# Kernel optimization log

Hardware: AMD Instinct MI355X
Metric: run time of the kernel (lower is better)

Reference implementation:

```python
import jax, jax.numpy as jnp
import numpy as np

D_MODEL = 1024
NUM_HEADS = 16
D_K = D_MODEL // NUM_HEADS
THETA = 10000.0
MAX_SEQ_LEN = 2048
BATCH = 2
SEQ = 2048


def setup_inputs() -> dict:
    key = jax.random.key(0)
    ks = jax.random.split(key, 5)
    std = np.sqrt(2.0 / (D_MODEL + D_MODEL)).astype(np.float32)
    x = jax.random.normal(ks[0], (BATCH, SEQ, D_MODEL), dtype=jnp.float32)
    Wq = jax.random.normal(ks[1], (D_MODEL, D_MODEL), dtype=jnp.float32) * std
    Wk = jax.random.normal(ks[2], (D_MODEL, D_MODEL), dtype=jnp.float32) * std
    Wv = jax.random.normal(ks[3], (D_MODEL, D_MODEL), dtype=jnp.float32) * std
    Wo = jax.random.normal(ks[4], (D_MODEL, D_MODEL), dtype=jnp.float32) * std
    token_positions = jnp.arange(SEQ, dtype=jnp.int32)
    return {"x": x, "token_positions": token_positions,
            "Wq": Wq, "Wk": Wk, "Wv": Wv, "Wo": Wo}


def _rope_tables(positions):
    # freqs: [d_k/2]; angles: [seq, d_k/2]
    freqs = 1.0 / (THETA ** (jnp.arange(0, D_K, 2, dtype=jnp.float32) / D_K))
    angles = positions.astype(jnp.float32)[:, None] * freqs[None, :]
    return jnp.cos(angles), jnp.sin(angles)


def _apply_rope(t, cos, sin):
    # t: [b, h, s, d_k]; cos/sin: [s, d_k/2]; interleaved pair rotation
    x1 = t[..., 0::2]
    x2 = t[..., 1::2]
    r1 = x1 * cos - x2 * sin
    r2 = x1 * sin + x2 * cos
    return jnp.stack([r1, r2], axis=-1).reshape(t.shape)


def reference(x, token_positions, Wq, Wk, Wv, Wo):
    b, s, _ = x.shape
    # projections: y = x W^T
    q = jnp.einsum('bsi,oi->bso', x, Wq)
    k = jnp.einsum('bsi,oi->bso', x, Wk)
    v = jnp.einsum('bsi,oi->bso', x, Wv)
    # split heads: [b, h, s, d]
    q = q.reshape(b, s, NUM_HEADS, D_K).transpose(0, 2, 1, 3)
    k = k.reshape(b, s, NUM_HEADS, D_K).transpose(0, 2, 1, 3)
    v = v.reshape(b, s, NUM_HEADS, D_K).transpose(0, 2, 1, 3)
    cos, sin = _rope_tables(token_positions)
    q = _apply_rope(q, cos, sin)
    k = _apply_rope(k, cos, sin)
    scale = jnp.asarray(D_K, jnp.float32) ** 0.5
    scores = jnp.einsum('bhqd,bhkd->bhqk', q, k) / scale
    causal = jnp.tril(jnp.ones((s, s), dtype=bool))
    scores = jnp.where(causal, scores, -jnp.inf)
    attn = jax.nn.softmax(scores.astype(jnp.float32), axis=-1).astype(scores.dtype)
    out = jnp.einsum('bhqk,bhkd->bhqd', attn, v)
    out = out.transpose(0, 2, 1, 3).reshape(b, s, D_MODEL)
    return jnp.einsum('bsi,oi->bso', out, Wo)
```

## Files before the change

kernel.cpp:

```cpp
#include <hip/hip_runtime.h>
#include <stdint.h>

#define D_MODEL 1024
#define NH      16
#define DKH     64
#define SEQLEN  2048
#define BATCH   2
#define KDIM    1024

typedef __attribute__((ext_vector_type(8))) short          short8;
typedef __attribute__((ext_vector_type(4))) short          bf16x4;
typedef __attribute__((ext_vector_type(8))) unsigned short ushort8;
typedef __attribute__((ext_vector_type(4))) unsigned short usht4;
typedef __attribute__((ext_vector_type(4))) float          f32x4;

#define QSCALE 0.18033688011112042f

__device__ __forceinline__ unsigned short f2bf(float f) {
    union { float f; unsigned u; } v; v.f = f;
    unsigned u = v.u;
    unsigned r = (u + 0x7FFFu + ((u >> 16) & 1u)) >> 16;
    return (unsigned short)r;
}
__device__ __forceinline__ unsigned fbits(float f) {
    union { float f; unsigned u; } v; v.f = f; return v.u;
}

__device__ __forceinline__ void gload_lds16(const unsigned short* g, unsigned short* l) {
    __builtin_amdgcn_global_load_lds(
        (__attribute__((address_space(1))) void*)(g),
        (__attribute__((address_space(3))) void*)(l), 16, 0, 0);
}

__global__ void cvt_all(const float* __restrict__ X,  const float* __restrict__ Wq,
                        const float* __restrict__ Wk, const float* __restrict__ Wv,
                        const float* __restrict__ Wo, const int* __restrict__ pos,
                        unsigned short* __restrict__ Xb,  unsigned short* __restrict__ Wqb,
                        unsigned short* __restrict__ Wkb, unsigned short* __restrict__ Wvb,
                        unsigned short* __restrict__ Wob, float2* __restrict__ tbl) {
    const int z = blockIdx.y;
    if (z == 5) {
        int i = blockIdx.x * 256 + threadIdx.x;
        if (i < 65536) {
            int s = i >> 5, j = i & 31;
            float freq = expf(-((float)(2 * j) * (1.0f / 64.0f)) * 9.210340371976184f);
            float ang = (float)pos[s] * freq;
            float sn, cn;
            sincosf(ang, &sn, &cn);
            tbl[i] = make_float2(cn, sn);
        }
        return;
    }
    const float* src; unsigned short* dst; int n;
    if (z == 0)      { src = X;  dst = Xb;  n = 4194304; }
    else if (z == 1) { src = Wq; dst = Wqb; n = 1048576; }
    else if (z == 2) { src = Wk; dst = Wkb; n = 1048576; }
    else if (z == 3) { src = Wv; dst = Wvb; n = 1048576; }
    else             { src = Wo; dst = Wob; n = 1048576; }
    int i = (blockIdx.x * 256 + threadIdx.x) * 8;
    if (i >= n) return;
    float4 a = *(const float4*)(src + i);
    float4 b = *(const float4*)(src + i + 4);
    ushort8 o;
    o[0] = f2bf(a.x); o[1] = f2bf(a.y); o[2] = f2bf(a.z); o[3] = f2bf(a.w);
    o[4] = f2bf(b.x); o[5] = f2bf(b.y); o[6] = f2bf(b.z); o[7] = f2bf(b.w);
    *(ushort8*)(dst + i) = o;
}

__device__ __forceinline__ void gemm_core_128(
    const unsigned short* __restrict__ A, const unsigned short* __restrict__ W,
    unsigned short* a_lds, unsigned short* b_lds,
    int m0, int n0, f32x4 acc[4][4])
{
    const int tid  = threadIdx.x;
    const int lane = tid & 63;
    const int w    = tid >> 6;
    const int quad = lane >> 4;
    const int l16  = lane & 15;
    const int wm   = w & 1, wn = w >> 1;

    const int row_in = lane >> 3;
    const int cg     = ((lane & 7) ^ row_in) * 8;

    #pragma unroll
    for (int mi = 0; mi < 4; mi++)
        #pragma unroll
        for (int ni = 0; ni < 4; ni++) {
            f32x4 z = {0.f, 0.f, 0.f, 0.f};
            acc[mi][ni] = z;
        }

    const int x7 = l16 & 7;

    for (int kk = 0; kk < KDIM; kk += 64) {
        __syncthreads();
        #pragma unroll
        for (int j = 0; j < 4; ++j) {
            int c = w * 4 + j;
            gload_lds16(A + (size_t)(m0 + c * 8 + row_in) * KDIM + kk + cg, &a_lds[c * 512]);
            gload_lds16(W + (size_t)(n0 + c * 8 + row_in) * KDIM + kk + cg, &b_lds[c * 512]);
        }
        __syncthreads();

        short8 af[2][4], bf[2][4];
        #pragma unroll
        for (int kk2 = 0; kk2 < 2; kk2++)
            #pragma unroll
            for (int i = 0; i < 4; i++) {
                int g = (kk2 * 4 + quad) ^ x7;
                af[kk2][i] = *(const short8*)&a_lds[(wm * 64 + i * 16 + l16) * 64 + g * 8];
                bf[kk2][i] = *(const short8*)&b_lds[(wn * 64 + i * 16 + l16) * 64 + g * 8];
            }
        #pragma unroll
        for (int kk2 = 0; kk2 < 2; kk2++)
            #pragma unroll
            for (int mi = 0; mi < 4; mi++)
                #pragma unroll
                for (int ni = 0; ni < 4; ni++)
                    acc[mi][ni] = __builtin_amdgcn_mfma_f32_16x16x32_bf16(af[kk2][mi], bf[kk2][ni], acc[mi][ni], 0, 0, 0);
    }
}

__global__ __launch_bounds__(256, 2)
void gemm_qkv(const unsigned short* __restrict__ X,
              const unsigned short* __restrict__ Wq,
              const unsigned short* __restrict__ Wk,
              const unsigned short* __restrict__ Wv,
              const float2* __restrict__ tbl,
              unsigned short* __restrict__ q_ws,
              unsigned short* __restrict__ k_ws,
              unsigned short* __restrict__ v_ws)
{
    __shared__ __align__(16) unsigned short a_lds[128 * 64];
    __shared__ __align__(16) unsigned short b_lds[128 * 64];
    __shared__ __align__(16) unsigned short t_lds[32 * 136];

    const int z = blockIdx.z;
    const unsigned short* W = (z == 0) ? Wq : ((z == 1) ? Wk : Wv);
    const int m0 = blockIdx.x * 128, n0 = blockIdx.y * 128;

    f32x4 acc[4][4];
    gemm_core_128(X, W, a_lds, b_lds, m0, n0, acc);

    const int tid  = threadIdx.x;
    const int lane = tid & 63;
    const int w    = tid >> 6;
    const int quad = lane >> 4;
    const int l16  = lane & 15;
    const int wm   = w & 1, wn = w >> 1;

    if (z == 2) {
        const int bx = m0 >> 11;
        const int c_local_w = wn * 16 + l16;
        const int rd_c = tid >> 3;
        const int rd_s = (tid & 7) * 16;
        #pragma unroll
        for (int ni = 0; ni < 4; ni++) {
            __syncthreads();
            #pragma unroll
            for (int mi = 0; mi < 4; mi++) {
                usht4 v4;
                #pragma unroll
                for (int r = 0; r < 4; r++) v4[r] = f2bf(acc[mi][ni][r]);
                *(usht4*)&t_lds[c_local_w * 136 + wm * 64 + mi * 16 + quad * 4] = v4;
            }
            __syncthreads();
            int col = n0 + (rd_c >> 4) * 64 + ni * 16 + (rd_c & 15);
            int h = col >> 6, d = col & 63;
            size_t base = (size_t)(bx * NH + h) * DKH * SEQLEN + (size_t)d * SEQLEN
                        + (m0 & 2047) + rd_s;
            ushort8 x0 = *(ushort8*)&t_lds[rd_c * 136 + rd_s];
            ushort8 x1 = *(ushort8*)&t_lds[rd_c * 136 + rd_s + 8];
            *(ushort8*)&v_ws[base]     = x0;
            *(ushort8*)&v_ws[base + 8] = x1;
        }
    } else {
        unsigned short* dst = (z == 0) ? q_ws : k_ws;
        const float sc = (z == 0) ? QSCALE : 1.0f;
        #pragma unroll
        for (int mi = 0; mi < 4; mi++)
            #pragma unroll
            for (int ni = 0; ni < 4; ni++)
                #pragma unroll
                for (int r = 0; r < 4; r++) {
                    int row = m0 + wm * 64 + mi * 16 + quad * 4 + r;
                    int col = n0 + wn * 64 + ni * 16 + l16;
                    int b = row >> 11, s = row & 2047;
                    int h = col >> 6,  d = col & 63;
                    float val = acc[mi][ni][r];
                    float other = __shfl_xor(val, 1);
                    float2 cs = tbl[s * 32 + (d >> 1)];
                    float rv = (d & 1) ? (other * cs.y + val * cs.x)
                                       : (val * cs.x - other * cs.y);
                    dst[(size_t)(b * NH + h) * SEQLEN * DKH + (size_t)s * DKH + d] =
                        f2bf(rv * sc);
                }
    }
}

__global__ __launch_bounds__(512, 2)
void attn_kernel(const unsigned short* __restrict__ q_ws,
                 const unsigned short* __restrict__ k_ws,
                 const unsigned short* __restrict__ v_ws,
                 unsigned short* __restrict__ ao)
{
    __shared__ __align__(16) unsigned short smem[17920];
    unsigned short* k_lds = smem;
    unsigned short* v_lds = smem + 128 * 72;
    float* redO = (float*)smem;
    float* redL = redO + 8192;

    const int bh  = blockIdx.x;
    const int y   = blockIdx.y;
    const int qt2 = (y < 8) ? y : (23 - y);
    const int tid = threadIdx.x, lane = tid & 63, w = tid >> 6;
    const int quad = lane >> 4, l16 = lane & 15;
    const int g   = w >> 2;
    const int w4  = w & 3;
    const int nf0 = g * 4;

    const size_t kqbase = (size_t)bh * SEQLEN * DKH;
    const size_t vbase  = (size_t)bh * DKH * SEQLEN;
    const int b = bh >> 4, h = bh & 15;

    const int krow = tid >> 3, kcol = (tid & 7) * 8;
    const int vrow = tid >> 4, vcol = (tid & 15) * 8;

    const int q0  = qt2 * 128;
    const int nt  = qt2 + 1;
    const int qwbase = q0 + w4 * 32;

    short8 aq[2][2];
    #pragma unroll
    for (int st = 0; st < 2; st++)
        #pragma unroll
        for (int kc = 0; kc < 2; kc++)
            aq[st][kc] = *(const short8*)(q_ws + kqbase +
                (size_t)(qwbase + st * 16 + l16) * DKH + kc * 32 + quad * 8);

    f32x4 o_acc[2][4];
    #pragma unroll
    for (int st = 0; st < 2; st++)
        #pragma unroll
        for (int df = 0; df < 4; df++) { f32x4 z = {0.f,0.f,0.f,0.f}; o_acc[st][df] = z; }
    float lsum[2] = {0.f, 0.f};

    ushort8 kreg[2], vreg[2];
    #pragma unroll
    for (int rr = 0; rr < 2; ++rr) {
        kreg[rr] = *(const ushort8*)(k_ws + kqbase + (size_t)(krow + rr * 64) * DKH + kcol);
        vreg[rr] = *(const ushort8*)(v_ws + vbase + (size_t)(vrow + rr * 32) * SEQLEN + vcol);
    }

    for (int t = 0; t < nt; ++t) {
        const int s0 = t * 128;
        __syncthreads();
        #pragma unroll
        for (int rr = 0; rr < 2; ++rr) {
            *(ushort8*)&k_lds[(krow + rr * 64) * 72 + kcol]  = kreg[rr];
            *(ushort8*)&v_lds[(vrow + rr * 32) * 136 + vcol] = vreg[rr];
        }
        __syncthreads();
        if (t < nt - 1) {
            int s1 = s0 + 128;
            #pragma unroll
            for (int rr = 0; rr < 2; ++rr) {
                kreg[rr] = *(const ushort8*)(k_ws + kqbase + (size_t)(s1 + krow + rr * 64) * DKH + kcol);
                vreg[rr] = *(const ushort8*)(v_ws + vbase + (size_t)(vrow + rr * 32) * SEQLEN + s1 + vcol);
            }
        }

        const bool diag = (t == nt - 1);
        #pragma unroll
        for (int nfi = 0; nfi < 4; nfi++) {
            const int nf = nf0 + nfi;
            short8 kf0 = *(const short8*)&k_lds[(nf * 16 + l16) * 72 + 0 * 32 + quad * 8];
            short8 kf1 = *(const short8*)&k_lds[(nf * 16 + l16) * 72 + 1 * 32 + quad * 8];
            bf16x4 vf[4];
            #pragma unroll
            for (int df = 0; df < 4; df++)
                vf[df] = *(const bf16x4*)&v_lds[(df * 16 + l16) * 136 + nf * 16 + quad * 4];

            #pragma unroll
            for (int st = 0; st < 2; st++) {
                f32x4 s = {0.f,0.f,0.f,0.f};
                s = __builtin_amdgcn_mfma_f32_16x16x32_bf16(kf0, aq[st][0], s, 0, 0, 0);
                s = __builtin_amdgcn_mfma_f32_16x16x32_bf16(kf1, aq[st][1], s, 0, 0, 0);

                if (diag) {
                    int qg = qwbase + st * 16 + l16;
                    int kg = s0 + nf * 16 + quad * 4;
                    #pragma unroll
                    for (int r = 0; r < 4; r++)
                        s[r] = (kg + r <= qg) ? __builtin_amdgcn_exp2f(s[r]) : 0.f;
                } else {
                    #pragma unroll
                    for (int r = 0; r < 4; r++)
                        s[r] = __builtin_amdgcn_exp2f(s[r]);
                }
                lsum[st] += s[0] + s[1] + s[2] + s[3];

                union { unsigned u[2]; bf16x4 v; } pk;
                pk.u[0] = __builtin_amdgcn_perm(fbits(s[1]), fbits(s[0]), 0x07060302u);
                pk.u[1] = __builtin_amdgcn_perm(fbits(s[3]), fbits(s[2]), 0x07060302u);

                #pragma unroll
                for (int df = 0; df < 4; df++)
                    o_acc[st][df] = __builtin_amdgcn_mfma_f32_16x16x16bf16_1k(vf[df], pk.v, o_acc[st][df], 0, 0, 0);
            }
        }
    }

    __syncthreads();
    if (g == 1) {
        #pragma unroll
        for (int st = 0; st < 2; st++) {
            #pragma unroll
            for (int df = 0; df < 4; df++)
                *(f32x4*)&redO[(((w4 * 2 + st) * 4 + df) << 8) + lane * 4] = o_acc[st][df];
            redL[(w4 * 2 + st) * 64 + lane] = lsum[st];
        }
    }
    __syncthreads();
    if (g == 0) {
        #pragma unroll
        for (int st = 0; st < 2; st++) {
            #pragma unroll
            for (int df = 0; df < 4; df++) {
                f32x4 o1 = *(const f32x4*)&redO[(((w4 * 2 + st) * 4 + df) << 8) + lane * 4];
                o_acc[st][df] += o1;
            }
            float rs = lsum[st] + redL[(w4 * 2 + st) * 64 + lane];
            rs += __shfl_xor(rs, 16);
            rs += __shfl_xor(rs, 32);
            float inv = 1.0f / rs;
            int qg = qwbase + st * 16 + l16;
            #pragma unroll
            for (int df = 0; df < 4; df++) {
                usht4 ov;
                #pragma unroll
                for (int r = 0; r < 4; r++) ov[r] = f2bf(o_acc[st][df][r] * inv);
                *(usht4*)&ao[(size_t)(b * SEQLEN + qg) * D_MODEL + h * DKH + df * 16 + quad * 4] = ov;
            }
        }
    }
}

__global__ __launch_bounds__(256, 2)
void gemm_out(const unsigned short* __restrict__ AO,
              const unsigned short* __restrict__ Wo,
              float* __restrict__ out)
{
    __shared__ __align__(16) unsigned short a_lds[128 * 64];
    __shared__ __align__(16) unsigned short b_lds[128 * 64];

    const int m0 = blockIdx.x * 128, n0 = blockIdx.y * 128;
    f32x4 acc[4][4];
    gemm_core_128(AO, Wo, a_lds, b_lds, m0, n0, acc);

    const int lane = threadIdx.x & 63;
    const int w    = threadIdx.x >> 6;
    const int quad = lane >> 4;
    const int l16  = lane & 15;
    const int wm   = w & 1, wn = w >> 1;

    #pragma unroll
    for (int mi = 0; mi < 4; mi++)
        #pragma unroll
        for (int ni = 0; ni < 4; ni++)
            #pragma unroll
            for (int r = 0; r < 4; r++) {
                int row = m0 + wm * 64 + mi * 16 + quad * 4 + r;
                int col = n0 + wn * 64 + ni * 16 + l16;
                out[(size_t)row * D_MODEL + col] = acc[mi][ni][r];
            }
}

extern "C" void kernel_launch(void* const* d_in, const int* in_sizes, int n_in,
                              void* d_out, int out_size, void* d_ws, size_t ws_size,
                              hipStream_t stream) {
    const float* X  = (const float*)d_in[0];
    const int*   pos = (const int*)d_in[1];
    const float* Wq = (const float*)d_in[2];
    const float* Wk = (const float*)d_in[3];
    const float* Wv = (const float*)d_in[4];
    const float* Wo = (const float*)d_in[5];
    float* out = (float*)d_out;

    unsigned short* Xb  = (unsigned short*)d_ws;
    unsigned short* Wqb = Xb + 4194304;
    unsigned short* Wkb = Wqb + 1048576;
    unsigned short* Wvb = Wkb + 1048576;
    unsigned short* Wob = Wvb + 1048576;
    unsigned short* q_ws = Wob + 1048576;
    unsigned short* k_ws = q_ws + 4194304;
    unsigned short* v_ws = k_ws + 4194304;
    unsigned short* ao   = v_ws + 4194304;
    float2* tbl = (float2*)(ao + 4194304);

    cvt_all<<<dim3(2048, 6), dim3(256), 0, stream>>>(X, Wq, Wk, Wv, Wo, pos,
                                                     Xb, Wqb, Wkb, Wvb, Wob, tbl);
    gemm_qkv<<<dim3(32, 8, 3), dim3(256), 0, stream>>>(Xb, Wqb, Wkb, Wvb, tbl, q_ws, k_ws, v_ws);
    attn_kernel<<<dim3(32, 16), dim3(512), 0, stream>>>(q_ws, k_ws, v_ws, ao);
    gemm_out<<<dim3(32, 8), dim3(256), 0, stream>>>(ao, Wob, out);
}
```

Measured before the change: 167.1 us.

## Double-buffer LDS tiles in shared GEMM core to overlap loads with MFMA

The GEMM core now keeps two LDS buffers for the A and W tiles. It loads the first tile before the loop, then issues the global-to-LDS load for the next K-slice before running the MFMAs on the current slice, with one barrier per iteration instead of two. The goal is to hide global load latency behind compute in both the QKV and output projection kernels. In exchange, LDS use per block doubles (about 64KB for the GEMM tiles), which could limit occupancy at two blocks per CU.

```diff
diff --git a/kernel.cpp b/kernel.cpp
--- a/kernel.cpp
+++ b/kernel.cpp
@@ -92,24 +92,38 @@
 
     const int x7 = l16 & 7;
 
+    #pragma unroll
+    for (int j = 0; j < 4; ++j) {
+        int c = w * 4 + j;
+        gload_lds16(A + (size_t)(m0 + c * 8 + row_in) * KDIM + cg, &a_lds[c * 512]);
+        gload_lds16(W + (size_t)(n0 + c * 8 + row_in) * KDIM + cg, &b_lds[c * 512]);
+    }
+    __syncthreads();
+
+    int cur = 0;
     for (int kk = 0; kk < KDIM; kk += 64) {
-        __syncthreads();
-        #pragma unroll
-        for (int j = 0; j < 4; ++j) {
-            int c = w * 4 + j;
-            gload_lds16(A + (size_t)(m0 + c * 8 + row_in) * KDIM + kk + cg, &a_lds[c * 512]);
-            gload_lds16(W + (size_t)(n0 + c * 8 + row_in) * KDIM + kk + cg, &b_lds[c * 512]);
-        }
-        __syncthreads();
-
+        if (kk + 64 < KDIM) {
+            const int nxt = cur ^ 1;
+            #pragma unroll
+            for (int j = 0; j < 4; ++j) {
+                int c = w * 4 + j;
+                gload_lds16(A + (size_t)(m0 + c * 8 + row_in) * KDIM + kk + 64 + cg,
+                            &a_lds[nxt * 8192 + c * 512]);
+                gload_lds16(W + (size_t)(n0 + c * 8 + row_in) * KDIM + kk + 64 + cg,
+                            &b_lds[nxt * 8192 + c * 512]);
+            }
+        }
+
+        const unsigned short* al = &a_lds[cur * 8192];
+        const unsigned short* bl = &b_lds[cur * 8192];
         short8 af[2][4], bf[2][4];
         #pragma unroll
         for (int kk2 = 0; kk2 < 2; kk2++)
             #pragma unroll
             for (int i = 0; i < 4; i++) {
                 int g = (kk2 * 4 + quad) ^ x7;
-                af[kk2][i] = *(const short8*)&a_lds[(wm * 64 + i * 16 + l16) * 64 + g * 8];
-                bf[kk2][i] = *(const short8*)&b_lds[(wn * 64 + i * 16 + l16) * 64 + g * 8];
+                af[kk2][i] = *(const short8*)&al[(wm * 64 + i * 16 + l16) * 64 + g * 8];
+                bf[kk2][i] = *(const short8*)&bl[(wn * 64 + i * 16 + l16) * 64 + g * 8];
             }
         #pragma unroll
         for (int kk2 = 0; kk2 < 2; kk2++)
@@ -118,6 +132,9 @@
                 #pragma unroll
                 for (int ni = 0; ni < 4; ni++)
                     acc[mi][ni] = __builtin_amdgcn_mfma_f32_16x16x32_bf16(af[kk2][mi], bf[kk2][ni], acc[mi][ni], 0, 0, 0);
+
+        __syncthreads();
+        cur ^= 1;
     }
 }
 
@@ -131,8 +148,8 @@
               unsigned short* __restrict__ k_ws,
               unsigned short* __restrict__ v_ws)
 {
-    __shared__ __align__(16) unsigned short a_lds[128 * 64];
-    __shared__ __align__(16) unsigned short b_lds[128 * 64];
+    __shared__ __align__(16) unsigned short a_lds[2 * 128 * 64];
+    __shared__ __align__(16) unsigned short b_lds[2 * 128 * 64];
     __shared__ __align__(16) unsigned short t_lds[32 * 136];
 
     const int z = blockIdx.z;
@@ -351,8 +368,8 @@
               const unsigned short* __restrict__ Wo,
               float* __restrict__ out)
 {
-    __shared__ __align__(16) unsigned short a_lds[128 * 64];
-    __shared__ __align__(16) unsigned short b_lds[128 * 64];
+    __shared__ __align__(16) unsigned short a_lds[2 * 128 * 64];
+    __shared__ __align__(16) unsigned short b_lds[2 * 128 * 64];
 
     const int m0 = blockIdx.x * 128, n0 = blockIdx.y * 128;
     f32x4 acc[4][4];
```

New measurement: 176.2 us. +5.4%, slower.
